# Kernel tuning notes

Measured on AMD Instinct MI355X. Metric: run time of the kernel, lower is better.

## Reference

```python
import jax, jax.numpy as jnp
import numpy as np

B, T, H, V = 256, 256, 512, 32000
L = 3  # stacked LSTM layers


def setup_inputs() -> dict:
    key = jax.random.key(0)
    ks = jax.random.split(key, 12)
    s = 0.05
    n = lambda k, shp: (jax.random.normal(k, shp, jnp.float32) * s)
    return {
        "text_1": jax.random.randint(ks[0], (B, T), 0, V, dtype=jnp.int32),
        "text_2": jax.random.randint(ks[1], (B, T), 0, V, dtype=jnp.int32),
        "text_3": jax.random.randint(ks[2], (B, T), 0, V, dtype=jnp.int32),
        "emb": n(ks[3], (V, H)),
        "Wx": n(ks[4], (L, H, 4 * H)),
        "Wh": n(ks[5], (L, H, 4 * H)),
        "b": jnp.zeros((L, 4 * H), jnp.float32),
        "g1": jnp.ones((3 * H,), jnp.float32), "beta1": jnp.zeros((3 * H,), jnp.float32),
        "W1": n(ks[6], (3 * H, 2 * H)), "bd1": jnp.zeros((2 * H,), jnp.float32),
        "g2": jnp.ones((2 * H,), jnp.float32), "beta2": jnp.zeros((2 * H,), jnp.float32),
        "W2": n(ks[7], (2 * H, H // 5)), "bd2": jnp.zeros((H // 5,), jnp.float32),
        "g3": jnp.ones((H // 5,), jnp.float32), "beta3": jnp.zeros((H // 5,), jnp.float32),
        "W3": n(ks[8], (H // 5, 4)), "bd3": jnp.zeros((4,), jnp.float32),
    }


def _lstm_stack(tokens, emb, Wx, Wh, b):
    # tokens: [B, T] int -> last hidden of top layer [B, H]
    x = emb[tokens]                      # [B, T, H]
    x = jnp.transpose(x, (1, 0, 2))      # [T, B, H] (scan over time)
    bsz, h = x.shape[1], Wh.shape[1]
    for l in range(Wx.shape[0]):
        Wx_l, Wh_l, b_l = Wx[l], Wh[l], b[l]
        def step(carry, xt):
            hprev, cprev = carry
            gates = xt @ Wx_l + hprev @ Wh_l + b_l      # [B, 4H]
            i, f, g, o = jnp.split(gates, 4, axis=-1)
            c = jax.nn.sigmoid(f) * cprev + jax.nn.sigmoid(i) * jnp.tanh(g)
            hnew = jax.nn.sigmoid(o) * jnp.tanh(c)
            return (hnew, c), hnew
        init = (jnp.zeros((bsz, h), x.dtype), jnp.zeros((bsz, h), x.dtype))
        _, x = jax.lax.scan(step, init, x)
    return x[-1]                          # rnn_output[:, -1, :]


def _bn(x, gamma, beta, eps=1e-3):
    m = jnp.mean(x, axis=0)
    v = jnp.var(x, axis=0)
    return gamma * (x - m) * jax.lax.rsqrt(v + eps) + beta


def reference(text_1, text_2, text_3, emb, Wx, Wh, b,
              g1, beta1, W1, bd1, g2, beta2, W2, bd2, g3, beta3, W3, bd3):
    r1 = _lstm_stack(text_1, emb, Wx, Wh, b)
    r2 = _lstm_stack(text_2, emb, Wx, Wh, b)
    r3 = _lstm_stack(text_3, emb, Wx, Wh, b)
    r = jnp.concatenate([r1, r2, r3], axis=1)   # [B, 3H]
    r = _bn(r, g1, beta1)
    r = jax.nn.selu(r @ W1 + bd1)
    r = _bn(r, g2, beta2)
    r = jax.nn.selu(r @ W2 + bd2)
    r = _bn(r, g3, beta3)
    return r @ W3 + bd3                          # [B, 4] logits
```

## Files before the change

kernel.cpp:

```cpp
#include <hip/hip_runtime.h>
#include <hip/hip_bf16.h>

typedef __attribute__((ext_vector_type(8))) short short8;
typedef __attribute__((ext_vector_type(4))) float floatx4;
typedef __attribute__((ext_vector_type(4))) unsigned uintx4;

namespace {
constexpr int kB1 = 256;
constexpr int kT  = 256;
constexpr int kH  = 512;
constexpr int kL  = 3;
constexpr int kB3 = 768;
constexpr int kK  = 1024;
constexpr int kN  = 2048;
constexpr int kV  = 32000;
constexpr size_t kHB = (size_t)kB3 * kH;
constexpr int kRing = 16;
constexpr int kFenceP = 12;

constexpr size_t WREP_OFF   = 0;
constexpr size_t WREP_BYTES = (size_t)kL * kK * kN * 2;
constexpr size_t BREP_OFF   = WREP_OFF + WREP_BYTES;
constexpr size_t BREP_BYTES = (size_t)kL * kN * 4;
constexpr size_t EMB_OFF    = BREP_OFF + BREP_BYTES;
constexpr size_t EMB_BYTES  = (size_t)kV * kH * 2;
constexpr size_t HBUF_OFF   = EMB_OFF + EMB_BYTES;
constexpr size_t HBUF_BYTES = (size_t)kL * kRing * kHB * 2;
constexpr size_t CBUF_OFF   = HBUF_OFF + HBUF_BYTES;
constexpr size_t CBUF_BYTES = (size_t)kL * kHB * 4;
constexpr size_t BNA_OFF    = CBUF_OFF + CBUF_BYTES;
constexpr size_t BNC_OFF    = BNA_OFF + 1536 * 4;
constexpr size_t Z1_OFF     = BNC_OFF + 1536 * 4;
constexpr size_t Z2_OFF     = Z1_OFF + (size_t)256 * 1024 * 4;
constexpr size_t FLAG_OFF   = Z2_OFF + (size_t)256 * 102 * 4;
constexpr size_t BAR_OFF    = FLAG_OFF + 128;
constexpr size_t WS_NEEDED  = BAR_OFF + 4096;
constexpr int kPersistGrid  = 768;
constexpr int kGenIdx       = 960;
}

__device__ __forceinline__ float ldf(const void* p, size_t idx, int isf32) {
  if (isf32) return ((const float*)p)[idx];
  return __bfloat162float(((const __hip_bfloat16*)p)[idx]);
}

__device__ __forceinline__ short f2bs(float x) {
  union { __hip_bfloat16 h; short s; } u;
  u.h = __float2bfloat16(x);
  return u.s;
}

__device__ __forceinline__ short8 cvt8(const float* q) {
  float4 lo = *(const float4*)q;
  float4 hi = *(const float4*)(q + 4);
  short8 v;
  v[0] = f2bs(lo.x); v[1] = f2bs(lo.y); v[2] = f2bs(lo.z); v[3] = f2bs(lo.w);
  v[4] = f2bs(hi.x); v[5] = f2bs(hi.y); v[6] = f2bs(hi.z); v[7] = f2bs(hi.w);
  return v;
}

__global__ void detect_kernel(const unsigned* __restrict__ g1, int* __restrict__ flag,
                              unsigned* __restrict__ bar) {
  int tid = threadIdx.x;
#pragma unroll
  for (int i = 0; i < 4; i++)
    __hip_atomic_store(&bar[tid + 256 * i], 0u, __ATOMIC_RELAXED, __HIP_MEMORY_SCOPE_AGENT);
  if (tid == 0 && blockIdx.x == 0)
    *flag = (g1[0] == 0x3F800000u) ? 1 : 0;
}

__global__ __launch_bounds__(256) void repack_kernel(
    const void* __restrict__ Wx, const void* __restrict__ Wh,
    const void* __restrict__ bias, const int* __restrict__ flagp,
    __hip_bfloat16* __restrict__ Wrep, float* __restrict__ brep) {
  int isf32 = *flagp;
  int idx = blockIdx.x * 256 + threadIdx.x;
  if (idx >= kL * kK * kN) return;
  int j  = idx & 7;
  int n2 = (idx >> 3) & (kN - 1);
  int kg = (idx >> 14) & 127;
  int l  = idx >> 21;
  int k  = kg * 8 + j;
  int ntile = n2 >> 7, c = n2 & 127, g = c >> 5, ul = c & 31;
  int u = ntile * 32 + ul;
  int col = g * 512 + u;
  float v;
  if (k < kH) v = ldf(Wx, ((size_t)l * kH + k) * kN + col, isf32);
  else        v = ldf(Wh, ((size_t)l * kH + (k - kH)) * kN + col, isf32);
  Wrep[idx] = __float2bfloat16(v);
  if (kg == 0 && j == 0) brep[l * kN + n2] = ldf(bias, (size_t)l * kN + col, isf32);
}

__global__ __launch_bounds__(256) void embrep_kernel(
    const void* __restrict__ emb, const int* __restrict__ flagp,
    __hip_bfloat16* __restrict__ er) {
  int isf32 = *flagp;
  size_t base = ((size_t)blockIdx.x * 256 + threadIdx.x) * 8;
  if (base >= (size_t)kV * kH) return;
  if (isf32) *(short8*)(er + base) = cvt8((const float*)emb + base);
  else       *(short8*)(er + base) = *(const short8*)((const __hip_bfloat16*)emb + base);
}

__device__ __forceinline__ void grid_barrier(unsigned* bar, int bid, int tid,
                                             unsigned sval, bool fence) {
  __syncthreads();
  if (tid == 0)
    __hip_atomic_store(&bar[bid], sval, __ATOMIC_RELEASE, __HIP_MEMORY_SCOPE_AGENT);
  if (bid == 0) {
    if (tid < 64) {
      const unsigned* fp = bar + (tid << 2);
      long long t0 = (long long)__builtin_amdgcn_s_memrealtime();
      int it = 0;
      for (;;) {
        uintx4 a, b, c;
        asm volatile("global_load_dwordx4 %0, %3, off sc0 sc1\n\t"
                     "global_load_dwordx4 %1, %4, off sc0 sc1\n\t"
                     "global_load_dwordx4 %2, %5, off sc0 sc1\n\t"
                     "s_waitcnt vmcnt(0)"
                     : "=v"(a), "=v"(b), "=v"(c)
                     : "v"(fp), "v"(fp + 256), "v"(fp + 512));
        bool ok = a[0] == sval && a[1] == sval && a[2] == sval && a[3] == sval &&
                  b[0] == sval && b[1] == sval && b[2] == sval && b[3] == sval &&
                  c[0] == sval && c[1] == sval && c[2] == sval && c[3] == sval;
        if (__all(ok)) break;
        __builtin_amdgcn_s_sleep(1);
        if (((++it) & 15) == 0 &&
            (long long)__builtin_amdgcn_s_memrealtime() - t0 > 20000000LL) break;
      }
      if (tid == 0)
        __hip_atomic_store(&bar[kGenIdx], sval, __ATOMIC_RELEASE, __HIP_MEMORY_SCOPE_AGENT);
    }
  } else if (tid == 0) {
    long long t0 = (long long)__builtin_amdgcn_s_memrealtime();
    int it = 0;
    while (__hip_atomic_load(&bar[kGenIdx], __ATOMIC_RELAXED, __HIP_MEMORY_SCOPE_AGENT) < sval) {
      __builtin_amdgcn_s_sleep(4);
      if (((++it) & 63) == 0 &&
          (long long)__builtin_amdgcn_s_memrealtime() - t0 > 20000000LL) break;
    }
  }
  __syncthreads();
  if (fence)
    __builtin_amdgcn_fence(__ATOMIC_ACQUIRE, "agent");
}

__global__ __launch_bounds__(256, 3) void persist_kernel(
    const __hip_bfloat16* __restrict__ Wrep, const float* __restrict__ brep,
    __hip_bfloat16* __restrict__ hbuf, const __hip_bfloat16* __restrict__ er,
    const int* __restrict__ flagp, const int* __restrict__ t1,
    const int* __restrict__ t2, const int* __restrict__ t3,
    unsigned* __restrict__ bar) {
  __shared__ __align__(16) char smem[26624];

  const int tid = threadIdx.x;
  const int bid = blockIdx.x;
  const int xcd = bid & 7;
  const int jj_ = bid >> 3;
  const int l   = jj_ >> 5;
  const int rr_ = jj_ & 31;
  const int cmb = (xcd - 3 * l) & 7;
  const int mt  = (cmb >> 2) * 8 + (rr_ >> 2);
  const int nt  = (cmb & 3) * 4 + (rr_ & 3);

  const int wv = tid >> 6, lane = tid & 63, lm = lane & 15, lq = lane >> 4;
  const int r0   = tid >> 4;
  const int c16  = tid & 15;
  const int kcol = c16 * 8;

  const int R0 = mt * 48 + r0, R1 = R0 + 16, R2 = R0 + 32;
  const int* tb0 = nullptr; const int* tb1 = nullptr; const int* tb2 = nullptr;
  int tk0 = 0, tk1 = 0, tk2 = 0;
  if (l == 0) {
    tb0 = (((R0 >> 8) == 0) ? t1 : ((R0 >> 8) == 1) ? t2 : t3) + (R0 & 255) * kT;
    tb1 = (((R1 >> 8) == 0) ? t1 : ((R1 >> 8) == 1) ? t2 : t3) + (R1 & 255) * kT;
    tb2 = (((R2 >> 8) == 0) ? t1 : ((R2 >> 8) == 1) ? t2 : t3) + (R2 & 255) * kT;
    tk0 = tb0[0]; tk1 = tb1[0]; tk2 = tb2[0];
  }
  const unsigned ro0 = (unsigned)R0 * kH + kcol;
  const unsigned ro1 = (unsigned)R1 * kH + kcol;
  const unsigned ro2 = (unsigned)R2 * kH + kcol;

  const __hip_bfloat16* WB = Wrep + (size_t)l * kK * kN;
  const int n0w = nt * 128 + wv * 32;
  const float bv0 = brep[l * kN + n0w + lm];
  const float bv1 = brep[l * kN + n0w + 16 + lm];

  char* aw0 = smem + r0 * 256 + ((c16 ^ (r0 & 7)) << 4);
  char* aw1 = aw0 + 16 * 256;
  char* aw2 = aw0 + 32 * 256;
  const char* arb = smem + lm * 256;
  int oswz[4];
#pragma unroll
  for (int kk = 0; kk < 4; kk++) oswz[kk] = (((kk * 4 + lq) ^ (lm & 7)) << 4);

  const int cuu = tid & 31, crow = tid >> 5;
  float creg[6] = {0.f, 0.f, 0.f, 0.f, 0.f, 0.f};

  short8 aA0, aA1, aA2, aB0, aB1, aB2;
  short8 bA[4][2], bB[4][2];
  const __hip_bfloat16 *xe0 = nullptr, *xe1 = nullptr, *xe2 = nullptr;
  if (l == 0) {
    xe0 = er + (size_t)tk0 * kH + kcol;
    xe1 = er + (size_t)tk1 * kH + kcol;
    xe2 = er + (size_t)tk2 * kH + kcol;
  }

#pragma unroll 1
  for (int s = 0; s < kT + kL - 1; s++) {
    const int t = s - l;
    if (t >= 0 && t < kT) {
      const __hip_bfloat16* hp = hbuf + ((size_t)l * kRing + ((t + kRing - 1) & (kRing - 1))) * kHB;
      const __hip_bfloat16* xh = nullptr;
      int nk0 = 0, nk1 = 0, nk2 = 0;
      if (l == 0) {
        if (t + 1 < kT) { nk0 = tb0[t + 1]; nk1 = tb1[t + 1]; nk2 = tb2[t + 1]; }
      } else {
        xh = hbuf + ((size_t)(l - 1) * kRing + (t & (kRing - 1))) * kHB;
      }

      auto loadA = [&](int sl, short8& d0, short8& d1, short8& d2) {
        if (sl < 4) {
          if (l == 0) {
            d0 = *(const short8*)(xe0 + sl * 128);
            d1 = *(const short8*)(xe1 + sl * 128);
            d2 = *(const short8*)(xe2 + sl * 128);
          } else {
            d0 = *(const short8*)(xh + ro0 + sl * 128);
            d1 = *(const short8*)(xh + ro1 + sl * 128);
            d2 = *(const short8*)(xh + ro2 + sl * 128);
          }
        } else if (t == 0) {
          short8 z = {0, 0, 0, 0, 0, 0, 0, 0};
          d0 = z; d1 = z; d2 = z;
        } else {
          d0 = *(const short8*)(hp + ro0 + (sl - 4) * 128);
          d1 = *(const short8*)(hp + ro1 + (sl - 4) * 128);
          d2 = *(const short8*)(hp + ro2 + (sl - 4) * 128);
        }
      };
      auto loadB = [&](int sl, short8 (&bf)[4][2]) {
#pragma unroll
        for (int kk = 0; kk < 4; kk++)
#pragma unroll
          for (int nf = 0; nf < 2; nf++) {
            int kg = sl * 16 + kk * 4 + lq;
            bf[kk][nf] = *(const short8*)(WB + ((size_t)kg * kN + n0w + nf * 16 + lm) * 8);
          }
      };

      if (l != 0 || t == 0) loadA(0, aA0, aA1, aA2);
      if (t == 0) loadB(0, bA);

      floatx4 zf = {0.f, 0.f, 0.f, 0.f};
      floatx4 acc[3][2];
#pragma unroll
      for (int a = 0; a < 3; a++) { acc[a][0] = zf; acc[a][1] = zf; }

#pragma unroll
      for (int sl = 0; sl < 8; sl++) {
        __syncthreads();
        if ((sl & 1) == 0) { *(short8*)aw0 = aA0; *(short8*)aw1 = aA1; *(short8*)aw2 = aA2; }
        else               { *(short8*)aw0 = aB0; *(short8*)aw1 = aB1; *(short8*)aw2 = aB2; }
        __syncthreads();
        if (sl < 7) {
          if ((sl & 1) == 0) { loadA(sl + 1, aB0, aB1, aB2); loadB(sl + 1, bB); }
          else               { loadA(sl + 1, aA0, aA1, aA2); loadB(sl + 1, bA); }
        }
#pragma unroll
        for (int kk = 0; kk < 4; kk++) {
          const short8* bf = (sl & 1) ? &bB[kk][0] : &bA[kk][0];
          short8 af0 = *(const short8*)(arb + 0 * 4096 + oswz[kk]);
          short8 af1 = *(const short8*)(arb + 1 * 4096 + oswz[kk]);
          short8 af2 = *(const short8*)(arb + 2 * 4096 + oswz[kk]);
          acc[0][0] = __builtin_amdgcn_mfma_f32_16x16x32_bf16(af0, bf[0], acc[0][0], 0, 0, 0);
          acc[0][1] = __builtin_amdgcn_mfma_f32_16x16x32_bf16(af0, bf[1], acc[0][1], 0, 0, 0);
          acc[1][0] = __builtin_amdgcn_mfma_f32_16x16x32_bf16(af1, bf[0], acc[1][0], 0, 0, 0);
          acc[1][1] = __builtin_amdgcn_mfma_f32_16x16x32_bf16(af1, bf[1], acc[1][1], 0, 0, 0);
          acc[2][0] = __builtin_amdgcn_mfma_f32_16x16x32_bf16(af2, bf[0], acc[2][0], 0, 0, 0);
          acc[2][1] = __builtin_amdgcn_mfma_f32_16x16x32_bf16(af2, bf[1], acc[2][1], 0, 0, 0);
        }
      }

      __syncthreads();
      float* gl = (float*)smem;
#pragma unroll
      for (int mf = 0; mf < 3; mf++)
#pragma unroll
        for (int nf = 0; nf < 2; nf++)
#pragma unroll
          for (int r = 0; r < 4; r++) {
            int rowf = mf * 16 + lq * 4 + r;
            gl[(wv * 48 + rowf) * 34 + nf * 16 + lm] = acc[mf][nf][r] + (nf ? bv1 : bv0);
          }
      __syncthreads();

      __hip_bfloat16* hout = hbuf + ((size_t)l * kRing + (t & (kRing - 1))) * kHB;
#pragma unroll
      for (int ii = 0; ii < 6; ii++) {
        int rowf = crow + 8 * ii;
        float gi = fminf(fmaxf(gl[(0 * 48 + rowf) * 34 + cuu], -40.f), 40.f);
        float gf = fminf(fmaxf(gl[(1 * 48 + rowf) * 34 + cuu], -40.f), 40.f);
        float gg = fminf(fmaxf(gl[(2 * 48 + rowf) * 34 + cuu], -40.f), 40.f);
        float go = fminf(fmaxf(gl[(3 * 48 + rowf) * 34 + cuu], -40.f), 40.f);
        float c_old = (t > 0) ? creg[ii] : 0.f;
        float si = 1.f / (1.f + __expf(-gi));
        float sf = 1.f / (1.f + __expf(-gf));
        float so = 1.f / (1.f + __expf(-go));
        float cn = sf * c_old + si * tanhf(gg);
        float hn = so * tanhf(cn);
        creg[ii] = cn;
        union { __hip_bfloat16 h; unsigned short u; } cv;
        cv.h = __float2bfloat16(hn);
        __hip_atomic_store(
            (unsigned short*)(hout + (size_t)(mt * 48 + rowf) * kH + nt * 32 + cuu),
            cv.u, __ATOMIC_RELAXED, __HIP_MEMORY_SCOPE_AGENT);
      }

      if (t + 1 < kT) {
        loadB(0, bA);
        if (l == 0) {
          tk0 = nk0; tk1 = nk1; tk2 = nk2;
          xe0 = er + (size_t)tk0 * kH + kcol;
          xe1 = er + (size_t)tk1 * kH + kcol;
          xe2 = er + (size_t)tk2 * kH + kcol;
          loadA(0, aA0, aA1, aA2);
        }
      }
    }
    if (s < kT + kL - 2)
      grid_barrier(bar, bid, tid, (unsigned)(s + 1), (s % kFenceP) == (kFenceP - 1));
  }
}

__global__ __launch_bounds__(256) void step_kernel(
    int s,
    const __hip_bfloat16* __restrict__ Wrep, const float* __restrict__ brep,
    __hip_bfloat16* __restrict__ hbuf, float* __restrict__ cbuf,
    const void* __restrict__ emb, const int* __restrict__ flagp,
    const int* __restrict__ t1, const int* __restrict__ t2, const int* __restrict__ t3) {
  __shared__ __align__(16) char smem[34816];

  int bid = blockIdx.x;
  int l  = bid / 192;
  int rr = bid % 192;
  int nt = rr & 15;
  int mt = rr >> 4;
  int t = s - l;
  if (t < 0 || t >= kT) return;

  int isf32 = *flagp;
  int tid = threadIdx.x;
  int wv = tid >> 6, lane = tid & 63;
  int lm = lane & 15, lq = lane >> 4;

  int arow = tid >> 2;
  int kc   = tid & 3;
  int row_g = mt * 64 + arow;

  const void* xsrc;
  bool xf32 = false;
  if (l == 0) {
    int i = row_g >> 8, bb = row_g & 255;
    const int* txt = (i == 0) ? t1 : (i == 1) ? t2 : t3;
    int tok = txt[bb * kT + t];
    if (isf32) { xsrc = (const void*)((const float*)emb + (size_t)tok * kH); xf32 = true; }
    else         xsrc = (const void*)((const __hip_bfloat16*)emb + (size_t)tok * kH);
  } else {
    const __hip_bfloat16* hIn = hbuf + ((size_t)(l - 1) * kRing + (t & (kRing - 1))) * kHB;
    xsrc = (const void*)(hIn + (size_t)row_g * kH);
  }
  const __hip_bfloat16* hrow = nullptr;
  if (t > 0) {
    const __hip_bfloat16* hPrev = hbuf + ((size_t)l * kRing + ((t + kRing - 1) & (kRing - 1))) * kHB;
    hrow = hPrev + (size_t)row_g * kH;
  }

  floatx4 zf = {0.f, 0.f, 0.f, 0.f};
  floatx4 acc[4][2];
#pragma unroll
  for (int a = 0; a < 4; a++)
#pragma unroll
    for (int b = 0; b < 2; b++) acc[a][b] = zf;

  const __hip_bfloat16* WB = Wrep + (size_t)l * kK * kN;
  int n0w = nt * 128 + wv * 32;

#pragma unroll 1
  for (int sl = 0; sl < 8; sl++) {
    short8 bfrag[4][2];
#pragma unroll
    for (int kk = 0; kk < 4; kk++)
#pragma unroll
      for (int nf = 0; nf < 2; nf++) {
        size_t kg = (size_t)(sl * 16 + kk * 4 + lq);
        const __hip_bfloat16* p = WB + (kg * kN + (n0w + nf * 16 + lm)) * 8;
        bfrag[kk][nf] = *(const short8*)p;
      }
    short8 av[4];
    bool zero = (sl >= 4) && (t == 0);
    if (!zero) {
      if (sl < 4 && xf32) {
        const float* sf = (const float*)xsrc + sl * 128;
#pragma unroll
        for (int jj = 0; jj < 4; jj++) {
          const float* q = sf + kc * 8 + jj * 32;
          float4 lo = *(const float4*)q;
          float4 hi = *(const float4*)(q + 4);
          short8 v;
          v[0] = f2bs(lo.x); v[1] = f2bs(lo.y); v[2] = f2bs(lo.z); v[3] = f2bs(lo.w);
          v[4] = f2bs(hi.x); v[5] = f2bs(hi.y); v[6] = f2bs(hi.z); v[7] = f2bs(hi.w);
          av[jj] = v;
        }
      } else {
        const __hip_bfloat16* src = (sl < 4)
            ? ((const __hip_bfloat16*)xsrc + sl * 128)
            : (hrow + (sl - 4) * 128);
#pragma unroll
        for (int jj = 0; jj < 4; jj++)
          av[jj] = *(const short8*)(src + kc * 8 + jj * 32);
      }
    } else {
      short8 vz = {0, 0, 0, 0, 0, 0, 0, 0};
#pragma unroll
      for (int jj = 0; jj < 4; jj++) av[jj] = vz;
    }
    __syncthreads();
#pragma unroll
    for (int jj = 0; jj < 4; jj++) {
      int klocal = kc * 8 + jj * 32;
      *(short8*)(smem + arow * 272 + klocal * 2) = av[jj];
    }
    __syncthreads();
#pragma unroll
    for (int kk = 0; kk < 4; kk++) {
      short8 afrag[4];
#pragma unroll
      for (int mf = 0; mf < 4; mf++) {
        int rowf = mf * 16 + lm;
        afrag[mf] = *(const short8*)(smem + rowf * 272 + kk * 64 + lq * 16);
      }
#pragma unroll
      for (int mf = 0; mf < 4; mf++)
#pragma unroll
        for (int nf = 0; nf < 2; nf++)
          acc[mf][nf] = __builtin_amdgcn_mfma_f32_16x16x32_bf16(
              afrag[mf], bfrag[kk][nf], acc[mf][nf], 0, 0, 0);
    }
  }

  const float* bl = brep + l * kN;
#pragma unroll
  for (int nf = 0; nf < 2; nf++) {
    float bv = bl[n0w + nf * 16 + lm];
#pragma unroll
    for (int mf = 0; mf < 4; mf++)
#pragma unroll
      for (int r = 0; r < 4; r++) acc[mf][nf][r] += bv;
  }

  __syncthreads();
  float* gl = (float*)smem;
#pragma unroll
  for (int mf = 0; mf < 4; mf++)
#pragma unroll
    for (int nf = 0; nf < 2; nf++)
#pragma unroll
      for (int r = 0; r < 4; r++) {
        int rowf = mf * 16 + lq * 4 + r;
        int uu   = nf * 16 + lm;
        gl[((size_t)wv * 64 + rowf) * 34 + uu] = acc[mf][nf][r];
      }
  __syncthreads();

  float* cl = cbuf + (size_t)l * kHB;
  __hip_bfloat16* hout = hbuf + ((size_t)l * kRing + (t & (kRing - 1))) * kHB;
#pragma unroll
  for (int ii = 0; ii < 8; ii++) {
    int idx = tid + 256 * ii;
    int uu = idx & 31, rowf = idx >> 5;
    float gi = fminf(fmaxf(gl[(0 * 64 + rowf) * 34 + uu], -40.f), 40.f);
    float gf = fminf(fmaxf(gl[(1 * 64 + rowf) * 34 + uu], -40.f), 40.f);
    float gg = fminf(fmaxf(gl[(2 * 64 + rowf) * 34 + uu], -40.f), 40.f);
    float go = fminf(fmaxf(gl[(3 * 64 + rowf) * 34 + uu], -40.f), 40.f);
    int bg = mt * 64 + rowf;
    int ug = nt * 32 + uu;
    size_t off = (size_t)bg * kH + ug;
    float c_old = (t > 0) ? cl[off] : 0.f;
    float si = 1.f / (1.f + __expf(-gi));
    float sf = 1.f / (1.f + __expf(-gf));
    float so = 1.f / (1.f + __expf(-go));
    float cn = sf * c_old + si * tanhf(gg);
    float hn = so * tanhf(cn);
    cl[off] = cn;
    hout[off] = __float2bfloat16(hn);
  }
}

__global__ __launch_bounds__(256) void stats_kernel(
    int ncols, int mode, const void* __restrict__ src,
    const void* __restrict__ gamma, const void* __restrict__ beta,
    const int* __restrict__ flagp, float* __restrict__ bn_a, float* __restrict__ bn_c) {
  int isf32 = *flagp;
  int col = blockIdx.x * 256 + threadIdx.x;
  if (col >= ncols) return;
  float sum = 0.f, ss = 0.f;
  for (int b = 0; b < kB1; b++) {
    float v;
    if (mode == 0) {
      const __hip_bfloat16* h = (const __hip_bfloat16*)src;
      v = __bfloat162float(h[((size_t)((col >> 9) * kB1 + b)) * kH + (col & 511)]);
    } else {
      v = ((const float*)src)[(size_t)b * ncols + col];
    }
    v = fmaxf(-1e15f, fminf(v, 1e15f));
    sum += v; ss += v * v;
  }
  float mean = sum * (1.f / kB1);
  float var  = ss * (1.f / kB1) - mean * mean;
  float a = ldf(gamma, col, isf32) * rsqrtf(var + 1e-3f);
  bn_a[col] = a;
  bn_c[col] = ldf(beta, col, isf32) - mean * a;
}

__global__ __launch_bounds__(256) void headgemm_kernel(
    int Kd, int Nd, int mode, const void* __restrict__ Asrc,
    const float* __restrict__ bn_a, const float* __restrict__ bn_c,
    const void* __restrict__ W, const void* __restrict__ bias,
    const int* __restrict__ flagp, float* __restrict__ out, int do_selu) {
  __shared__ float As[32][65];
  __shared__ float Bs[32][65];
  int isf32 = *flagp;
  int tid = threadIdx.x;
  int bx = blockIdx.x, by = blockIdx.y;
  int tx = tid & 15, ty = tid >> 4;
  float acc[4][4] = {};
  int am = tid & 63, ak = tid >> 6;
  int bk = tid >> 3, bn8 = (tid & 7) * 8;
  for (int ks = 0; ks < Kd; ks += 32) {
    __syncthreads();
    for (int jj = 0; jj < 8; jj++) {
      int kl = ak * 8 + jj;
      int kg = ks + kl;
      int mg = by * 64 + am;
      float v;
      if (mode == 0) {
        const __hip_bfloat16* h = (const __hip_bfloat16*)Asrc;
        v = __bfloat162float(h[((size_t)((kg >> 9) * kB1 + mg)) * kH + (kg & 511)]);
      } else {
        v = ((const float*)Asrc)[(size_t)mg * Kd + kg];
      }
      As[kl][am] = v * bn_a[kg] + bn_c[kg];
    }
    for (int e = 0; e < 8; e++) {
      int col = bx * 64 + bn8 + e;
      Bs[bk][bn8 + e] = (col < Nd) ? ldf(W, (size_t)(ks + bk) * Nd + col, isf32) : 0.f;
    }
    __syncthreads();
    for (int k = 0; k < 32; k++) {
      float ar[4], br[4];
#pragma unroll
      for (int i = 0; i < 4; i++) ar[i] = As[k][ty * 4 + i];
#pragma unroll
      for (int j = 0; j < 4; j++) br[j] = Bs[k][tx * 4 + j];
#pragma unroll
      for (int i = 0; i < 4; i++)
#pragma unroll
        for (int j = 0; j < 4; j++) acc[i][j] += ar[i] * br[j];
    }
  }
  for (int i = 0; i < 4; i++) {
    int row = by * 64 + ty * 4 + i;
    for (int j = 0; j < 4; j++) {
      int col = bx * 64 + tx * 4 + j;
      if (col < Nd) {
        float y = acc[i][j] + ldf(bias, col, isf32);
        if (do_selu)
          y = (y > 0.f) ? 1.0507009873554805f * y
                        : 1.0507009873554805f * 1.6732632423543772f * (__expf(y) - 1.f);
        out[(size_t)row * Nd + col] = y;
      }
    }
  }
}

__global__ __launch_bounds__(256) void final_kernel(
    const float* __restrict__ z2, const float* __restrict__ bn_a, const float* __restrict__ bn_c,
    const void* __restrict__ W3, const void* __restrict__ bd3,
    const int* __restrict__ flagp, void* __restrict__ out) {
  int isf32 = *flagp;
  int b = threadIdx.x;
  float acc[4] = {0.f, 0.f, 0.f, 0.f};
  for (int j = 0; j < 102; j++) {
    float y = z2[b * 102 + j] * bn_a[j] + bn_c[j];
#pragma unroll
    for (int g = 0; g < 4; g++) acc[g] += y * ldf(W3, j * 4 + g, isf32);
  }
#pragma unroll
  for (int g = 0; g < 4; g++) {
    float y = acc[g] + ldf(bd3, g, isf32);
    if (isf32) ((float*)out)[b * 4 + g] = y;
    else ((__hip_bfloat16*)out)[b * 4 + g] = __float2bfloat16(y);
  }
}

extern "C" void kernel_launch(void* const* d_in, const int* in_sizes, int n_in,
                              void* d_out, int out_size, void* d_ws, size_t ws_size,
                              hipStream_t stream) {
  const int* t1 = (const int*)d_in[0];
  const int* t2 = (const int*)d_in[1];
  const int* t3 = (const int*)d_in[2];
  const void* emb = d_in[3];
  const void* Wx  = d_in[4];
  const void* Wh  = d_in[5];
  const void* bb  = d_in[6];
  const void* g1  = d_in[7];
  const void* be1 = d_in[8];
  const void* W1  = d_in[9];
  const void* bd1 = d_in[10];
  const void* g2  = d_in[11];
  const void* be2 = d_in[12];
  const void* W2  = d_in[13];
  const void* bd2 = d_in[14];
  const void* g3  = d_in[15];
  const void* be3 = d_in[16];
  const void* W3  = d_in[17];
  const void* bd3 = d_in[18];

  char* ws = (char*)d_ws;
  __hip_bfloat16* Wrep = (__hip_bfloat16*)(ws + WREP_OFF);
  float* brep = (float*)(ws + BREP_OFF);
  __hip_bfloat16* embrep = (__hip_bfloat16*)(ws + EMB_OFF);
  __hip_bfloat16* hbuf = (__hip_bfloat16*)(ws + HBUF_OFF);
  float* cbuf = (float*)(ws + CBUF_OFF);
  float* bn_a = (float*)(ws + BNA_OFF);
  float* bn_c = (float*)(ws + BNC_OFF);
  float* z1 = (float*)(ws + Z1_OFF);
  float* z2 = (float*)(ws + Z2_OFF);
  int* flag = (int*)(ws + FLAG_OFF);
  unsigned* bar = (unsigned*)(ws + BAR_OFF);

  static int persist_ok = -1;
  if (persist_ok < 0) {
    int nb = 0, ncu = 0, dev = 0;
    (void)hipGetDevice(&dev);
    (void)hipDeviceGetAttribute(&ncu, hipDeviceAttributeMultiprocessorCount, dev);
    hipError_t e = hipOccupancyMaxActiveBlocksPerMultiprocessor(&nb, persist_kernel, 256, 0);
    persist_ok = (e == hipSuccess && (long)nb * (long)ncu >= kPersistGrid &&
                  ws_size >= WS_NEEDED) ? 1 : 0;
  }

  detect_kernel<<<1, 256, 0, stream>>>((const unsigned*)g1, flag, bar);

  repack_kernel<<<(kL * kK * kN) / 256, 256, 0, stream>>>(Wx, Wh, bb, flag, Wrep, brep);
  embrep_kernel<<<(kV * kH) / (256 * 8), 256, 0, stream>>>(emb, flag, embrep);

  if (persist_ok) {
    persist_kernel<<<kPersistGrid, 256, 0, stream>>>(
        Wrep, brep, hbuf, embrep, flag, t1, t2, t3, bar);
  } else {
    for (int s = 0; s < kT + kL - 1; s++)
      step_kernel<<<3 * 192, 256, 0, stream>>>(s, Wrep, brep, hbuf, cbuf, emb, flag, t1, t2, t3);
  }

  const __hip_bfloat16* hTop = hbuf + (size_t)(2 * kRing + ((kT - 1) & (kRing - 1))) * kHB;
  stats_kernel<<<6, 256, 0, stream>>>(1536, 0, hTop, g1, be1, flag, bn_a, bn_c);
  headgemm_kernel<<<dim3(16, 4), 256, 0, stream>>>(1536, 1024, 0, hTop, bn_a, bn_c, W1, bd1, flag, z1, 1);
  stats_kernel<<<4, 256, 0, stream>>>(1024, 1, z1, g2, be2, flag, bn_a, bn_c);
  headgemm_kernel<<<dim3(2, 4), 256, 0, stream>>>(1024, 102, 1, z1, bn_a, bn_c, W2, bd2, flag, z2, 1);
  stats_kernel<<<1, 256, 0, stream>>>(102, 1, z2, g3, be3, flag, bn_a, bn_c);
  final_kernel<<<1, 256, 0, stream>>>(z2, bn_a, bn_c, W3, bd3, flag, (void*)d_out);
}
```

Baseline: 6.101 ms.

## Use 192 persistent 1024-thread blocks with larger tiles and double-buffered LDS

Restructures the persistent LSTM kernel from 768 blocks of 256 threads into 192 blocks of 1024 threads, each owning a 96x256 output tile. The per-step grid barrier now tracks far fewer blocks, so the barrier poll reads one vector instead of three. The K loop becomes 16 phases over a double-buffered LDS A tile with a single sync per phase, and the starting phase is rotated between block halves. The intent is to cut grid-barrier latency and per-step synchronisation. In exchange each block does more work on fewer CUs and register pressure rises at 1024 threads.

After: 6.062 ms. Within noise of the previous version (-0.6%).

```diff
diff --git a/kernel.cpp b/kernel.cpp
--- a/kernel.cpp
+++ b/kernel.cpp
@@ -35,7 +35,7 @@
 constexpr size_t FLAG_OFF   = Z2_OFF + (size_t)256 * 102 * 4;
 constexpr size_t BAR_OFF    = FLAG_OFF + 128;
 constexpr size_t WS_NEEDED  = BAR_OFF + 4096;
-constexpr int kPersistGrid  = 768;
+constexpr int kPersistGrid  = 192;
 constexpr int kGenIdx       = 960;
 }
 
@@ -108,20 +108,15 @@
     __hip_atomic_store(&bar[bid], sval, __ATOMIC_RELEASE, __HIP_MEMORY_SCOPE_AGENT);
   if (bid == 0) {
     if (tid < 64) {
-      const unsigned* fp = bar + (tid << 2);
+      const unsigned* fp = bar + ((tid < 48) ? (tid << 2) : 0);
       long long t0 = (long long)__builtin_amdgcn_s_memrealtime();
       int it = 0;
       for (;;) {
-        uintx4 a, b, c;
-        asm volatile("global_load_dwordx4 %0, %3, off sc0 sc1\n\t"
-                     "global_load_dwordx4 %1, %4, off sc0 sc1\n\t"
-                     "global_load_dwordx4 %2, %5, off sc0 sc1\n\t"
+        uintx4 a;
+        asm volatile("global_load_dwordx4 %0, %1, off sc0 sc1\n\t"
                      "s_waitcnt vmcnt(0)"
-                     : "=v"(a), "=v"(b), "=v"(c)
-                     : "v"(fp), "v"(fp + 256), "v"(fp + 512));
-        bool ok = a[0] == sval && a[1] == sval && a[2] == sval && a[3] == sval &&
-                  b[0] == sval && b[1] == sval && b[2] == sval && b[3] == sval &&
-                  c[0] == sval && c[1] == sval && c[2] == sval && c[3] == sval;
+                     : "=v"(a) : "v"(fp));
+        bool ok = a[0] == sval && a[1] == sval && a[2] == sval && a[3] == sval;
         if (__all(ok)) break;
         __builtin_amdgcn_s_sleep(1);
         if (((++it) & 15) == 0 &&
@@ -144,66 +139,59 @@
     __builtin_amdgcn_fence(__ATOMIC_ACQUIRE, "agent");
 }
 
-__global__ __launch_bounds__(256, 3) void persist_kernel(
+__global__ __launch_bounds__(1024) void persist_kernel(
     const __hip_bfloat16* __restrict__ Wrep, const float* __restrict__ brep,
     __hip_bfloat16* __restrict__ hbuf, const __hip_bfloat16* __restrict__ er,
     const int* __restrict__ flagp, const int* __restrict__ t1,
     const int* __restrict__ t2, const int* __restrict__ t3,
     unsigned* __restrict__ bar) {
-  __shared__ __align__(16) char smem[26624];
+  __shared__ __align__(16) char smem[24576 + 4 * 96 * 66 * 4];
+  float* gl = (float*)(smem + 24576);
 
   const int tid = threadIdx.x;
   const int bid = blockIdx.x;
   const int xcd = bid & 7;
-  const int jj_ = bid >> 3;
-  const int l   = jj_ >> 5;
-  const int rr_ = jj_ & 31;
-  const int cmb = (xcd - 3 * l) & 7;
-  const int mt  = (cmb >> 2) * 8 + (rr_ >> 2);
-  const int nt  = (cmb & 3) * 4 + (rr_ & 3);
+  const int j_  = bid >> 3;
+  const int l   = j_ >> 3;
+  const int r_  = j_ & 7;
+  const int c_  = (xcd + 5 * l) & 7;
+  const int mt  = (c_ >> 2) * 4 + (r_ & 3);
+  const int nt  = (c_ & 3) * 2 + (r_ >> 2);
+  const int rot = (r_ >> 2) * 8;
 
   const int wv = tid >> 6, lane = tid & 63, lm = lane & 15, lq = lane >> 4;
-  const int r0   = tid >> 4;
-  const int c16  = tid & 15;
-  const int kcol = c16 * 8;
-
-  const int R0 = mt * 48 + r0, R1 = R0 + 16, R2 = R0 + 32;
-  const int* tb0 = nullptr; const int* tb1 = nullptr; const int* tb2 = nullptr;
-  int tk0 = 0, tk1 = 0, tk2 = 0;
-  if (l == 0) {
-    tb0 = (((R0 >> 8) == 0) ? t1 : ((R0 >> 8) == 1) ? t2 : t3) + (R0 & 255) * kT;
-    tb1 = (((R1 >> 8) == 0) ? t1 : ((R1 >> 8) == 1) ? t2 : t3) + (R1 & 255) * kT;
-    tb2 = (((R2 >> 8) == 0) ? t1 : ((R2 >> 8) == 1) ? t2 : t3) + (R2 & 255) * kT;
-    tk0 = tb0[0]; tk1 = tb1[0]; tk2 = tb2[0];
-  }
-  const unsigned ro0 = (unsigned)R0 * kH + kcol;
-  const unsigned ro1 = (unsigned)R1 * kH + kcol;
-  const unsigned ro2 = (unsigned)R2 * kH + kcol;
+  const int mrow = (wv >> 3) * 48;
+  const int ncol = nt * 256 + (wv & 7) * 32;
+
+  const int r0 = tid >> 3;
+  const int c8 = tid & 7;
+  const bool stg = (tid < 768);
+  const int R  = mt * 96 + r0;
+  const unsigned ro = (unsigned)R * kH + c8 * 8;
+
+  const int* tb = nullptr;
+  int tk = 0;
+  if (l == 0 && stg) {
+    tb = (((R >> 8) == 0) ? t1 : ((R >> 8) == 1) ? t2 : t3) + (R & 255) * kT;
+    tk = tb[0];
+  }
 
   const __hip_bfloat16* WB = Wrep + (size_t)l * kK * kN;
-  const int n0w = nt * 128 + wv * 32;
-  const float bv0 = brep[l * kN + n0w + lm];
-  const float bv1 = brep[l * kN + n0w + 16 + lm];
-
-  char* aw0 = smem + r0 * 256 + ((c16 ^ (r0 & 7)) << 4);
-  char* aw1 = aw0 + 16 * 256;
-  char* aw2 = aw0 + 32 * 256;
-  const char* arb = smem + lm * 256;
-  int oswz[4];
-#pragma unroll
-  for (int kk = 0; kk < 4; kk++) oswz[kk] = (((kk * 4 + lq) ^ (lm & 7)) << 4);
-
-  const int cuu = tid & 31, crow = tid >> 5;
+  const float bv0 = brep[l * kN + ncol + lm];
+  const float bv1 = brep[l * kN + ncol + 16 + lm];
+
+  char* aw = smem + r0 * 128 + ((c8 ^ (r0 & 7)) << 4);
+  int oswz[2];
+#pragma unroll
+  for (int kk = 0; kk < 2; kk++) oswz[kk] = (((kk * 4 + lq) ^ (lm & 7)) << 4);
+
+  const int cuu = tid & 63, crb = tid >> 6;
   float creg[6] = {0.f, 0.f, 0.f, 0.f, 0.f, 0.f};
 
-  short8 aA0, aA1, aA2, aB0, aB1, aB2;
-  short8 bA[4][2], bB[4][2];
-  const __hip_bfloat16 *xe0 = nullptr, *xe1 = nullptr, *xe2 = nullptr;
-  if (l == 0) {
-    xe0 = er + (size_t)tk0 * kH + kcol;
-    xe1 = er + (size_t)tk1 * kH + kcol;
-    xe2 = er + (size_t)tk2 * kH + kcol;
-  }
+  short8 aCur, aNxt;
+  short8 bA[2][2], bB[2][2];
+  const __hip_bfloat16* xe = nullptr;
+  if (l == 0 && stg) xe = er + (size_t)tk * kH + c8 * 8;
 
 #pragma unroll 1
   for (int s = 0; s < kT + kL - 1; s++) {
@@ -211,45 +199,37 @@
     if (t >= 0 && t < kT) {
       const __hip_bfloat16* hp = hbuf + ((size_t)l * kRing + ((t + kRing - 1) & (kRing - 1))) * kHB;
       const __hip_bfloat16* xh = nullptr;
-      int nk0 = 0, nk1 = 0, nk2 = 0;
+      int nk = 0;
       if (l == 0) {
-        if (t + 1 < kT) { nk0 = tb0[t + 1]; nk1 = tb1[t + 1]; nk2 = tb2[t + 1]; }
+        if (stg && t + 1 < kT) nk = tb[t + 1];
       } else {
         xh = hbuf + ((size_t)(l - 1) * kRing + (t & (kRing - 1))) * kHB;
       }
 
-      auto loadA = [&](int sl, short8& d0, short8& d1, short8& d2) {
-        if (sl < 4) {
-          if (l == 0) {
-            d0 = *(const short8*)(xe0 + sl * 128);
-            d1 = *(const short8*)(xe1 + sl * 128);
-            d2 = *(const short8*)(xe2 + sl * 128);
-          } else {
-            d0 = *(const short8*)(xh + ro0 + sl * 128);
-            d1 = *(const short8*)(xh + ro1 + sl * 128);
-            d2 = *(const short8*)(xh + ro2 + sl * 128);
-          }
+      auto loadA = [&](int p, short8& d) {
+        if (!stg) return;
+        if (p < 8) {
+          if (l == 0) d = *(const short8*)(xe + p * 64);
+          else        d = *(const short8*)(xh + ro + p * 64);
         } else if (t == 0) {
           short8 z = {0, 0, 0, 0, 0, 0, 0, 0};
-          d0 = z; d1 = z; d2 = z;
+          d = z;
         } else {
-          d0 = *(const short8*)(hp + ro0 + (sl - 4) * 128);
-          d1 = *(const short8*)(hp + ro1 + (sl - 4) * 128);
-          d2 = *(const short8*)(hp + ro2 + (sl - 4) * 128);
+          d = *(const short8*)(hp + ro + (p - 8) * 64);
         }
       };
-      auto loadB = [&](int sl, short8 (&bf)[4][2]) {
-#pragma unroll
-        for (int kk = 0; kk < 4; kk++)
+      auto loadB = [&](int p, short8 (&bf)[2][2]) {
+#pragma unroll
+        for (int kk = 0; kk < 2; kk++)
 #pragma unroll
           for (int nf = 0; nf < 2; nf++) {
-            int kg = sl * 16 + kk * 4 + lq;
-            bf[kk][nf] = *(const short8*)(WB + ((size_t)kg * kN + n0w + nf * 16 + lm) * 8);
+            int kg = p * 8 + kk * 4 + lq;
+            bf[kk][nf] = *(const short8*)(WB + ((size_t)kg * kN + ncol + nf * 16 + lm) * 8);
           }
       };
 
-      if (l != 0 || t == 0) loadA(0, aA0, aA1, aA2);
-      if (t == 0) loadB(0, bA);
+      if (t == 0 || l != 0 || rot >= 8) loadA(rot, aCur);
+      if (t == 0) loadB(rot, bA);
 
       floatx4 zf = {0.f, 0.f, 0.f, 0.f};
       floatx4 acc[3][2];
@@ -257,21 +237,22 @@
       for (int a = 0; a < 3; a++) { acc[a][0] = zf; acc[a][1] = zf; }
 
 #pragma unroll
-      for (int sl = 0; sl < 8; sl++) {
+      for (int si = 0; si < 16; si++) {
+        const int buf = si & 1;
+        if (stg) *(short8*)(aw + buf * 12288) = aCur;
         __syncthreads();
-        if ((sl & 1) == 0) { *(short8*)aw0 = aA0; *(short8*)aw1 = aA1; *(short8*)aw2 = aA2; }
-        else               { *(short8*)aw0 = aB0; *(short8*)aw1 = aB1; *(short8*)aw2 = aB2; }
-        __syncthreads();
-        if (sl < 7) {
-          if ((sl & 1) == 0) { loadA(sl + 1, aB0, aB1, aB2); loadB(sl + 1, bB); }
-          else               { loadA(sl + 1, aA0, aA1, aA2); loadB(sl + 1, bA); }
+        if (si < 15) {
+          const int pn = (si + 1 + rot) & 15;
+          loadA(pn, aNxt);
+          if (buf == 0) loadB(pn, bB); else loadB(pn, bA);
         }
-#pragma unroll
-        for (int kk = 0; kk < 4; kk++) {
-          const short8* bf = (sl & 1) ? &bB[kk][0] : &bA[kk][0];
-          short8 af0 = *(const short8*)(arb + 0 * 4096 + oswz[kk]);
-          short8 af1 = *(const short8*)(arb + 1 * 4096 + oswz[kk]);
-          short8 af2 = *(const short8*)(arb + 2 * 4096 + oswz[kk]);
+        const char* arb = smem + buf * 12288 + lm * 128;
+#pragma unroll
+        for (int kk = 0; kk < 2; kk++) {
+          const short8* bf = buf ? &bB[kk][0] : &bA[kk][0];
+          short8 af0 = *(const short8*)(arb + (mrow + 0) * 128 + oswz[kk]);
+          short8 af1 = *(const short8*)(arb + (mrow + 16) * 128 + oswz[kk]);
+          short8 af2 = *(const short8*)(arb + (mrow + 32) * 128 + oswz[kk]);
           acc[0][0] = __builtin_amdgcn_mfma_f32_16x16x32_bf16(af0, bf[0], acc[0][0], 0, 0, 0);
           acc[0][1] = __builtin_amdgcn_mfma_f32_16x16x32_bf16(af0, bf[1], acc[0][1], 0, 0, 0);
           acc[1][0] = __builtin_amdgcn_mfma_f32_16x16x32_bf16(af1, bf[0], acc[1][0], 0, 0, 0);
@@ -279,29 +260,33 @@
           acc[2][0] = __builtin_amdgcn_mfma_f32_16x16x32_bf16(af2, bf[0], acc[2][0], 0, 0, 0);
           acc[2][1] = __builtin_amdgcn_mfma_f32_16x16x32_bf16(af2, bf[1], acc[2][1], 0, 0, 0);
         }
-      }
-
-      __syncthreads();
-      float* gl = (float*)smem;
+        aCur = aNxt;
+        if (buf) {
+        }
+      }
+
 #pragma unroll
       for (int mf = 0; mf < 3; mf++)
 #pragma unroll
         for (int nf = 0; nf < 2; nf++)
 #pragma unroll
           for (int r = 0; r < 4; r++) {
-            int rowf = mf * 16 + lq * 4 + r;
-            gl[(wv * 48 + rowf) * 34 + nf * 16 + lm] = acc[mf][nf][r] + (nf ? bv1 : bv0);
+            int rowf = mrow + mf * 16 + lq * 4 + r;
+            int ct = (wv & 7) * 32 + nf * 16 + lm;
+            int ut = ct >> 7, cc = ct & 127;
+            int g = cc >> 5, ul = ut * 32 + (cc & 31);
+            gl[((size_t)g * 96 + rowf) * 66 + ul] = acc[mf][nf][r] + (nf ? bv1 : bv0);
           }
       __syncthreads();
 
       __hip_bfloat16* hout = hbuf + ((size_t)l * kRing + (t & (kRing - 1))) * kHB;
 #pragma unroll
       for (int ii = 0; ii < 6; ii++) {
-        int rowf = crow + 8 * ii;
-        float gi = fminf(fmaxf(gl[(0 * 48 + rowf) * 34 + cuu], -40.f), 40.f);
-        float gf = fminf(fmaxf(gl[(1 * 48 + rowf) * 34 + cuu], -40.f), 40.f);
-        float gg = fminf(fmaxf(gl[(2 * 48 + rowf) * 34 + cuu], -40.f), 40.f);
-        float go = fminf(fmaxf(gl[(3 * 48 + rowf) * 34 + cuu], -40.f), 40.f);
+        int rowf = crb + 16 * ii;
+        float gi = fminf(fmaxf(gl[(0 * 96 + rowf) * 66 + cuu], -40.f), 40.f);
+        float gf = fminf(fmaxf(gl[(1 * 96 + rowf) * 66 + cuu], -40.f), 40.f);
+        float gg = fminf(fmaxf(gl[(2 * 96 + rowf) * 66 + cuu], -40.f), 40.f);
+        float go = fminf(fmaxf(gl[(3 * 96 + rowf) * 66 + cuu], -40.f), 40.f);
         float c_old = (t > 0) ? creg[ii] : 0.f;
         float si = 1.f / (1.f + __expf(-gi));
         float sf = 1.f / (1.f + __expf(-gf));
@@ -312,18 +297,16 @@
         union { __hip_bfloat16 h; unsigned short u; } cv;
         cv.h = __float2bfloat16(hn);
         __hip_atomic_store(
-            (unsigned short*)(hout + (size_t)(mt * 48 + rowf) * kH + nt * 32 + cuu),
+            (unsigned short*)(hout + (size_t)(mt * 96 + rowf) * kH + nt * 64 + cuu),
             cv.u, __ATOMIC_RELAXED, __HIP_MEMORY_SCOPE_AGENT);
       }
 
       if (t + 1 < kT) {
-        loadB(0, bA);
-        if (l == 0) {
-          tk0 = nk0; tk1 = nk1; tk2 = nk2;
-          xe0 = er + (size_t)tk0 * kH + kcol;
-          xe1 = er + (size_t)tk1 * kH + kcol;
-          xe2 = er + (size_t)tk2 * kH + kcol;
-          loadA(0, aA0, aA1, aA2);
+        loadB(rot, bA);
+        if (l == 0 && stg) {
+          tk = nk;
+          xe = er + (size_t)tk * kH + c8 * 8;
+          if (rot < 8) loadA(rot, aCur);
         }
       }
     }
@@ -644,7 +627,7 @@
     int nb = 0, ncu = 0, dev = 0;
     (void)hipGetDevice(&dev);
     (void)hipDeviceGetAttribute(&ncu, hipDeviceAttributeMultiprocessorCount, dev);
-    hipError_t e = hipOccupancyMaxActiveBlocksPerMultiprocessor(&nb, persist_kernel, 256, 0);
+    hipError_t e = hipOccupancyMaxActiveBlocksPerMultiprocessor(&nb, persist_kernel, 1024, 0);
     persist_ok = (e == hipSuccess && (long)nb * (long)ncu >= kPersistGrid &&
                   ws_size >= WS_NEEDED) ? 1 : 0;
   }
@@ -655,7 +638,7 @@
   embrep_kernel<<<(kV * kH) / (256 * 8), 256, 0, stream>>>(emb, flag, embrep);
 
   if (persist_ok) {
-    persist_kernel<<<kPersistGrid, 256, 0, stream>>>(
+    persist_kernel<<<kPersistGrid, 1024, 0, stream>>>(
         Wrep, brep, hbuf, embrep, flag, t1, t2, t3, bar);
   } else {
     for (int s = 0; s < kT + kL - 1; s++)
```
